# Optimization experiments

Measured on AMD Instinct MI355X. Metric: run time of the kernel, lower is better.

## Reference

```python
import jax, jax.numpy as jnp
import numpy as np

N = 50000      # nodes
E = 800000     # edges (avg degree 16)
IN_DIM = 128
H = 8          # num_heads
D = 16         # out_dim per head


def setup_inputs() -> dict:
    key = jax.random.key(0)
    ks = jax.random.split(key, 10)
    s = 1.0 / np.sqrt(IN_DIM)
    return {
        "h_src": jax.random.normal(ks[0], (N, IN_DIM), jnp.float32),
        "h_dst": jax.random.normal(ks[1], (N, IN_DIM), jnp.float32),
        "src": jax.random.randint(ks[2], (E,), 0, N),
        "dst": jax.random.randint(ks[3], (E,), 0, N),
        "Qw": jax.random.normal(ks[4], (IN_DIM, H * D), jnp.float32) * s,
        "Qb": jnp.zeros((H * D,), jnp.float32),
        "Kw": jax.random.normal(ks[5], (IN_DIM, H * D), jnp.float32) * s,
        "Kb": jnp.zeros((H * D,), jnp.float32),
        "Vw": jax.random.normal(ks[6], (IN_DIM, H * D), jnp.float32) * s,
        "Vb": jnp.zeros((H * D,), jnp.float32),
    }


def reference(h_src, h_dst, src, dst, Qw, Qb, Kw, Kb, Vw, Vb):
    # Node-level projections: [N, H, D]
    Q = (h_dst @ Qw + Qb).reshape(-1, H, D)
    K = (h_src @ Kw + Kb).reshape(-1, H, D)
    V = (h_src @ Vw + Vb).reshape(-1, H, D)
    # Edge-wise dot product per head: [E, H, 1]
    score = jnp.sum(K[src] * Q[dst], axis=-1, keepdims=True)
    # exp of clamped scaled score (note: clamp(-5,5) BEFORE exp, as in scaled_exp)
    score = jnp.exp(jnp.clip(score / jnp.float32(np.sqrt(D)), -5.0, 5.0))
    # Scatter-sum aggregation onto destination nodes
    wV = jax.ops.segment_sum(score * V[src], dst, num_segments=N)  # [N, H, D]
    z = jax.ops.segment_sum(score, dst, num_segments=N)            # [N, H, 1]
    return wV / z
```

## Files before the change

kernel.cpp:

```cpp
#include <hip/hip_runtime.h>
#include <hip/hip_bf16.h>
#include <math.h>

#define N_NODES 50000
#define E_EDGES 800000
#define IN_DIM  128
#define HD      128
#define SQRT_D_INV 0.25f

#define HIST_BLOCKS 1024
#define PROJ_BLOCKS ((N_NODES + 63) / 64)

typedef __attribute__((ext_vector_type(8))) short short8v;
typedef __attribute__((ext_vector_type(4))) float float4v;

__device__ inline unsigned short f2bf(float x) {
    __hip_bfloat16 b = __float2bfloat16(x);
    return *reinterpret_cast<unsigned short*>(&b);
}
__device__ inline float bflo(unsigned int u) { return __uint_as_float(u << 16); }
__device__ inline float bfhi(unsigned int u) { return __uint_as_float(u & 0xffff0000u); }

__global__ __launch_bounds__(256) void wtr_init_kernel(
    const float* __restrict__ Qw, const float* __restrict__ Kw, const float* __restrict__ Vw,
    unsigned short* __restrict__ wt, int* __restrict__ counts8)
{
    int i = blockIdx.x * 256 + threadIdx.x;
    for (int j = i; j <= 8 * N_NODES; j += 392 * 256) counts8[j] = 0;
    if (i < 3 * 16384) {
        int which = i >> 14;
        int r = i & 16383;
        int k = r >> 7, n = r & 127;
        const float* W = (which == 0) ? Qw : (which == 1) ? Kw : Vw;
        wt[((size_t)which << 14) + n * 128 + k] = f2bf(W[r]);
    }
}

__global__ __launch_bounds__(256) void proj_hist_kernel(
    const float* __restrict__ h_src, const float* __restrict__ h_dst,
    const unsigned short* __restrict__ wt,
    const float* __restrict__ Qb, const float* __restrict__ Kb, const float* __restrict__ Vb,
    unsigned short* __restrict__ qkv,
    const int* __restrict__ dst, int* __restrict__ counts8, int* __restrict__ rank)
{
    if (blockIdx.x < HIST_BLOCKS) {
        const int c = blockIdx.x & 7;
        int* cnt = counts8 + c * N_NODES;
        int tid = blockIdx.x * 256 + threadIdx.x;
        for (int e = tid; e < E_EDGES; e += HIST_BLOCKS * 256)
            rank[e] = atomicAdd(&cnt[dst[e]], 1);
        return;
    }

    __shared__ __align__(16) unsigned short smem[16384];
    const int t  = threadIdx.x;
    const int wv = t >> 6;
    const int l  = t & 63;
    const int lr = l & 15;
    const int kg = l >> 4;
    const int m_base = (blockIdx.x - HIST_BLOCKS) * 64 + wv * 16;
    const int arow = min(m_base + lr, N_NODES - 1);

    const float* pd = h_dst + (size_t)arow * IN_DIM;
    const float* ps = h_src + (size_t)arow * IN_DIM;

    short8v afd[4], afs[4];
    #pragma unroll
    for (int ks = 0; ks < 4; ++ks) {
        const int k0 = ks * 32 + kg * 8;
        float4 a0 = *(const float4*)&pd[k0];
        float4 a1 = *(const float4*)&pd[k0 + 4];
        float4 b0 = *(const float4*)&ps[k0];
        float4 b1 = *(const float4*)&ps[k0 + 4];
        afd[ks][0] = (short)f2bf(a0.x); afd[ks][1] = (short)f2bf(a0.y);
        afd[ks][2] = (short)f2bf(a0.z); afd[ks][3] = (short)f2bf(a0.w);
        afd[ks][4] = (short)f2bf(a1.x); afd[ks][5] = (short)f2bf(a1.y);
        afd[ks][6] = (short)f2bf(a1.z); afd[ks][7] = (short)f2bf(a1.w);
        afs[ks][0] = (short)f2bf(b0.x); afs[ks][1] = (short)f2bf(b0.y);
        afs[ks][2] = (short)f2bf(b0.z); afs[ks][3] = (short)f2bf(b0.w);
        afs[ks][4] = (short)f2bf(b1.x); afs[ks][5] = (short)f2bf(b1.y);
        afs[ks][6] = (short)f2bf(b1.z); afs[ks][7] = (short)f2bf(b1.w);
    }

    unsigned short* stg = &smem[wv * 2176];

    #pragma unroll
    for (int phase = 0; phase < 3; ++phase) {
        if (phase) __syncthreads();
        const unsigned short* wsrc = wt + ((size_t)phase << 14);
        #pragma unroll
        for (int j = 0; j < 8; ++j) {
            const int selem = j * 2048 + t * 8;
            const int d = selem * 2;
            const int sd = d ^ (((d >> 8) & 15) << 4);
            *(short8v*)((char*)smem + sd) = *(const short8v*)&wsrc[selem];
        }
        __syncthreads();

        const short8v* aF = (phase == 0) ? afd : afs;
        float4v acc[8];
        #pragma unroll
        for (int i = 0; i < 8; ++i) acc[i] = (float4v)0.f;
        #pragma unroll
        for (int ks = 0; ks < 4; ++ks) {
            short8v bf[8];
            #pragma unroll
            for (int nf = 0; nf < 8; ++nf) {
                const int a = (nf * 16 + lr) * 256 + ks * 64 + kg * 16;
                const int sa = a ^ (lr << 4);
                bf[nf] = *(const short8v*)((const char*)smem + sa);
            }
            #pragma unroll
            for (int nf = 0; nf < 8; ++nf)
                acc[nf] = __builtin_amdgcn_mfma_f32_16x16x32_bf16(aF[ks], bf[nf], acc[nf], 0, 0, 0);
        }
        __syncthreads();

        const float* bias = (phase == 0) ? Qb : (phase == 1) ? Kb : Vb;
        #pragma unroll
        for (int nf = 0; nf < 8; ++nf) {
            const float b = bias[nf * 16 + lr];
            #pragma unroll
            for (int r = 0; r < 4; ++r)
                stg[(kg * 4 + r) * 136 + nf * 16 + lr] = f2bf(acc[nf][r] + b);
        }
        #pragma unroll
        for (int i = 0; i < 4; ++i) {
            const int chunk = i * 64 + l;
            const int row = chunk >> 4;
            const int c   = (chunk & 15) * 8;
            const int m = m_base + row;
            short8v v = *(const short8v*)&stg[row * 136 + c];
            if (m < N_NODES) *(short8v*)&qkv[(size_t)m * 384 + phase * 128 + c] = v;
        }
    }
}

__global__ __launch_bounds__(256) void offsets_kernel(const int* __restrict__ counts8,
                                                      int* __restrict__ begc,
                                                      int* __restrict__ begn,
                                                      int* __restrict__ cntn,
                                                      int* __restrict__ total) {
    int n = blockIdx.x * blockDim.x + threadIdx.x;
    int lane = threadIdx.x & 63;
    int pre[8];
    int s = 0;
    if (n < N_NODES) {
        #pragma unroll
        for (int c = 0; c < 8; ++c) {
            int v = counts8[c * N_NODES + n];
            pre[c] = s; s += v;
        }
    }
    int incl = s;
    #pragma unroll
    for (int off = 1; off < 64; off <<= 1) {
        int y = __shfl_up(incl, off);
        if (lane >= off) incl += y;
    }
    int wsum = __shfl(incl, 63);
    int base = 0;
    if (lane == 0) base = atomicAdd(total, wsum);
    base = __shfl(base, 0);
    int b = base + incl - s;
    if (n < N_NODES) {
        begn[n] = b; cntn[n] = s;
        #pragma unroll
        for (int c = 0; c < 8; ++c) begc[c * N_NODES + n] = b + pre[c];
    }
}

__global__ void scatter_kernel(const int* __restrict__ src, const int* __restrict__ dst,
                               const int* __restrict__ begc, const int* __restrict__ rank,
                               int* __restrict__ esrc) {
    int e = blockIdx.x * blockDim.x + threadIdx.x;
    if (e < E_EDGES) {
        int c = (e >> 8) & 7;
        esrc[begc[c * N_NODES + dst[e]] + rank[e]] = src[e];
    }
}

__global__ __launch_bounds__(256) void agg_kernel(
    const unsigned short* __restrict__ qkv,
    const int* __restrict__ begp, const int* __restrict__ cntp,
    const int* __restrict__ esrc, float* __restrict__ out)
{
    int wave = (blockIdx.x * blockDim.x + threadIdx.x) >> 6;
    const int lane = threadIdx.x & 63;
    if (wave >= N_NODES) return;
    const int n = __builtin_amdgcn_readfirstlane(wave);
    const int e = lane >> 4;
    const int u = lane & 15;

    const uint4 qv = *(const uint4*)&qkv[(size_t)n * 384 + u * 8];
    const float q0 = bflo(qv.x), q1 = bfhi(qv.x), q2 = bflo(qv.y), q3 = bfhi(qv.y);
    const float q4 = bflo(qv.z), q5 = bfhi(qv.z), q6 = bflo(qv.w), q7 = bfhi(qv.w);

    const int b0 = begp[n], c0 = cntp[n], endp = b0 + c0;

    float a0=0.f,a1=0.f,a2=0.f,a3=0.f,a4=0.f,a5=0.f,a6=0.f,a7=0.f, z=0.f;

    for (int base = b0; base < endp; base += 16) {
        int idx[4];
        uint4 kk[4], vv[4];
        #pragma unroll
        for (int j = 0; j < 4; ++j) {
            idx[j] = base + j * 4 + e;
            const int s = esrc[min(idx[j], endp - 1)];
            const size_t ro = (size_t)s * 384;
            kk[j] = *(const uint4*)&qkv[ro + 128 + u * 8];
            vv[j] = *(const uint4*)&qkv[ro + 256 + u * 8];
        }
        #pragma unroll
        for (int j = 0; j < 4; ++j) {
            float d =      q0 * bflo(kk[j].x);
            d = fmaf(q1, bfhi(kk[j].x), d);
            d = fmaf(q2, bflo(kk[j].y), d);
            d = fmaf(q3, bfhi(kk[j].y), d);
            d = fmaf(q4, bflo(kk[j].z), d);
            d = fmaf(q5, bfhi(kk[j].z), d);
            d = fmaf(q6, bflo(kk[j].w), d);
            d = fmaf(q7, bfhi(kk[j].w), d);
            d += __shfl_xor(d, 1);
            float w = (idx[j] < endp) ? __expf(fminf(fmaxf(d * SQRT_D_INV, -5.f), 5.f)) : 0.f;
            z += w;
            a0 = fmaf(w, bflo(vv[j].x), a0);
            a1 = fmaf(w, bfhi(vv[j].x), a1);
            a2 = fmaf(w, bflo(vv[j].y), a2);
            a3 = fmaf(w, bfhi(vv[j].y), a3);
            a4 = fmaf(w, bflo(vv[j].z), a4);
            a5 = fmaf(w, bfhi(vv[j].z), a5);
            a6 = fmaf(w, bflo(vv[j].w), a6);
            a7 = fmaf(w, bfhi(vv[j].w), a7);
        }
    }

    #pragma unroll
    for (int mask = 16; mask <= 32; mask <<= 1) {
        z  += __shfl_xor(z, mask);
        a0 += __shfl_xor(a0, mask);
        a1 += __shfl_xor(a1, mask);
        a2 += __shfl_xor(a2, mask);
        a3 += __shfl_xor(a3, mask);
        a4 += __shfl_xor(a4, mask);
        a5 += __shfl_xor(a5, mask);
        a6 += __shfl_xor(a6, mask);
        a7 += __shfl_xor(a7, mask);
    }

    const float inv = 1.f / z;
    if (e == 0) {
        *(float4*)&out[(size_t)n * HD + u * 8]     = make_float4(a0*inv, a1*inv, a2*inv, a3*inv);
        *(float4*)&out[(size_t)n * HD + u * 8 + 4] = make_float4(a4*inv, a5*inv, a6*inv, a7*inv);
    }
}

extern "C" void kernel_launch(void* const* d_in, const int* in_sizes, int n_in,
                              void* d_out, int out_size, void* d_ws, size_t ws_size,
                              hipStream_t stream) {
    const float* h_src = (const float*)d_in[0];
    const float* h_dst = (const float*)d_in[1];
    const int*   src   = (const int*)d_in[2];
    const int*   dst   = (const int*)d_in[3];
    const float* Qw    = (const float*)d_in[4];
    const float* Qb    = (const float*)d_in[5];
    const float* Kw    = (const float*)d_in[6];
    const float* Kb    = (const float*)d_in[7];
    const float* Vw    = (const float*)d_in[8];
    const float* Vb    = (const float*)d_in[9];
    float* out = (float*)d_out;

    char* ws = (char*)d_ws;
    const size_t qkv_bytes = (size_t)N_NODES * 384 * sizeof(unsigned short);
    const size_t wt_bytes  = 3 * 128 * 128 * sizeof(unsigned short);
    unsigned short* qkvp = (unsigned short*)(ws);
    unsigned short* wtp  = (unsigned short*)(ws + qkv_bytes);
    int* counts8 = (int*)(ws + qkv_bytes + wt_bytes);
    int* total   = counts8 + 8 * N_NODES;
    int* begc    = counts8 + 8 * N_NODES + 1;
    int* begn    = begc + 8 * N_NODES;
    int* cntn    = begn + N_NODES;
    int* rank    = cntn + N_NODES;
    int* esrc    = rank + E_EDGES;

    wtr_init_kernel<<<392, 256, 0, stream>>>(Qw, Kw, Vw, wtp, counts8);

    proj_hist_kernel<<<HIST_BLOCKS + PROJ_BLOCKS, 256, 0, stream>>>(
        h_src, h_dst, wtp, Qb, Kb, Vb, qkvp, dst, counts8, rank);

    offsets_kernel<<<(N_NODES + 255) / 256, 256, 0, stream>>>(counts8, begc, begn, cntn, total);

    scatter_kernel<<<(E_EDGES + 255) / 256, 256, 0, stream>>>(src, dst, begc, rank, esrc);

    agg_kernel<<<(N_NODES * 64 + 255) / 256, 256, 0, stream>>>(qkvp, begn, cntn, esrc, out);
}
```

Measured before the change: 138.1 us.

## Split Q/K/V projection phases across separate blocks instead of one block looping

Each projection block now computes only one of Q, K or V for its 64-row tile, tripling the projection grid instead of looping over three phases inside one block. This removes the serial phase loop and its extra barriers, adds parallelism and lets weight loads for different matrices overlap across blocks. In exchange, h_src rows are loaded twice (once each by the K and V blocks), and more blocks must be scheduled alongside the histogram blocks.

```diff
diff --git a/kernel.cpp b/kernel.cpp
--- a/kernel.cpp
+++ b/kernel.cpp
@@ -9,7 +9,8 @@
 #define SQRT_D_INV 0.25f
 
 #define HIST_BLOCKS 1024
-#define PROJ_BLOCKS ((N_NODES + 63) / 64)
+#define NT_TILES    ((N_NODES + 63) / 64)
+#define PROJ_BLOCKS (NT_TILES * 3)
 
 typedef __attribute__((ext_vector_type(8))) short short8v;
 typedef __attribute__((ext_vector_type(4))) float float4v;
@@ -53,86 +54,77 @@
     }
 
     __shared__ __align__(16) unsigned short smem[16384];
+    const int pb    = blockIdx.x - HIST_BLOCKS;
+    const int which = pb % 3;
+    const int tile  = pb / 3;
     const int t  = threadIdx.x;
     const int wv = t >> 6;
     const int l  = t & 63;
     const int lr = l & 15;
     const int kg = l >> 4;
-    const int m_base = (blockIdx.x - HIST_BLOCKS) * 64 + wv * 16;
+    const int m_base = tile * 64 + wv * 16;
     const int arow = min(m_base + lr, N_NODES - 1);
 
-    const float* pd = h_dst + (size_t)arow * IN_DIM;
-    const float* ps = h_src + (size_t)arow * IN_DIM;
-
-    short8v afd[4], afs[4];
+    const float* A  = (which == 0) ? h_dst : h_src;
+    const float* ap = A + (size_t)arow * IN_DIM;
+
+    short8v af[4];
     #pragma unroll
     for (int ks = 0; ks < 4; ++ks) {
         const int k0 = ks * 32 + kg * 8;
-        float4 a0 = *(const float4*)&pd[k0];
-        float4 a1 = *(const float4*)&pd[k0 + 4];
-        float4 b0 = *(const float4*)&ps[k0];
-        float4 b1 = *(const float4*)&ps[k0 + 4];
-        afd[ks][0] = (short)f2bf(a0.x); afd[ks][1] = (short)f2bf(a0.y);
-        afd[ks][2] = (short)f2bf(a0.z); afd[ks][3] = (short)f2bf(a0.w);
-        afd[ks][4] = (short)f2bf(a1.x); afd[ks][5] = (short)f2bf(a1.y);
-        afd[ks][6] = (short)f2bf(a1.z); afd[ks][7] = (short)f2bf(a1.w);
-        afs[ks][0] = (short)f2bf(b0.x); afs[ks][1] = (short)f2bf(b0.y);
-        afs[ks][2] = (short)f2bf(b0.z); afs[ks][3] = (short)f2bf(b0.w);
-        afs[ks][4] = (short)f2bf(b1.x); afs[ks][5] = (short)f2bf(b1.y);
-        afs[ks][6] = (short)f2bf(b1.z); afs[ks][7] = (short)f2bf(b1.w);
-    }
-
+        float4 a0 = *(const float4*)&ap[k0];
+        float4 a1 = *(const float4*)&ap[k0 + 4];
+        af[ks][0] = (short)f2bf(a0.x); af[ks][1] = (short)f2bf(a0.y);
+        af[ks][2] = (short)f2bf(a0.z); af[ks][3] = (short)f2bf(a0.w);
+        af[ks][4] = (short)f2bf(a1.x); af[ks][5] = (short)f2bf(a1.y);
+        af[ks][6] = (short)f2bf(a1.z); af[ks][7] = (short)f2bf(a1.w);
+    }
+
+    const unsigned short* wsrc = wt + ((size_t)which << 14);
+    #pragma unroll
+    for (int j = 0; j < 8; ++j) {
+        const int selem = j * 2048 + t * 8;
+        const int d = selem * 2;
+        const int sd = d ^ (((d >> 8) & 15) << 4);
+        *(short8v*)((char*)smem + sd) = *(const short8v*)&wsrc[selem];
+    }
+    __syncthreads();
+
+    float4v acc[8];
+    #pragma unroll
+    for (int i = 0; i < 8; ++i) acc[i] = (float4v)0.f;
+    #pragma unroll
+    for (int ks = 0; ks < 4; ++ks) {
+        short8v bf[8];
+        #pragma unroll
+        for (int nf = 0; nf < 8; ++nf) {
+            const int a = (nf * 16 + lr) * 256 + ks * 64 + kg * 16;
+            const int sa = a ^ (lr << 4);
+            bf[nf] = *(const short8v*)((const char*)smem + sa);
+        }
+        #pragma unroll
+        for (int nf = 0; nf < 8; ++nf)
+            acc[nf] = __builtin_amdgcn_mfma_f32_16x16x32_bf16(af[ks], bf[nf], acc[nf], 0, 0, 0);
+    }
+    __syncthreads();
+
+    const float* bias = (which == 0) ? Qb : (which == 1) ? Kb : Vb;
     unsigned short* stg = &smem[wv * 2176];
-
-    #pragma unroll
-    for (int phase = 0; phase < 3; ++phase) {
-        if (phase) __syncthreads();
-        const unsigned short* wsrc = wt + ((size_t)phase << 14);
-        #pragma unroll
-        for (int j = 0; j < 8; ++j) {
-            const int selem = j * 2048 + t * 8;
-            const int d = selem * 2;
-            const int sd = d ^ (((d >> 8) & 15) << 4);
-            *(short8v*)((char*)smem + sd) = *(const short8v*)&wsrc[selem];
-        }
-        __syncthreads();
-
-        const short8v* aF = (phase == 0) ? afd : afs;
-        float4v acc[8];
-        #pragma unroll
-        for (int i = 0; i < 8; ++i) acc[i] = (float4v)0.f;
-        #pragma unroll
-        for (int ks = 0; ks < 4; ++ks) {
-            short8v bf[8];
-            #pragma unroll
-            for (int nf = 0; nf < 8; ++nf) {
-                const int a = (nf * 16 + lr) * 256 + ks * 64 + kg * 16;
-                const int sa = a ^ (lr << 4);
-                bf[nf] = *(const short8v*)((const char*)smem + sa);
-            }
-            #pragma unroll
-            for (int nf = 0; nf < 8; ++nf)
-                acc[nf] = __builtin_amdgcn_mfma_f32_16x16x32_bf16(aF[ks], bf[nf], acc[nf], 0, 0, 0);
-        }
-        __syncthreads();
-
-        const float* bias = (phase == 0) ? Qb : (phase == 1) ? Kb : Vb;
-        #pragma unroll
-        for (int nf = 0; nf < 8; ++nf) {
-            const float b = bias[nf * 16 + lr];
-            #pragma unroll
-            for (int r = 0; r < 4; ++r)
-                stg[(kg * 4 + r) * 136 + nf * 16 + lr] = f2bf(acc[nf][r] + b);
-        }
-        #pragma unroll
-        for (int i = 0; i < 4; ++i) {
-            const int chunk = i * 64 + l;
-            const int row = chunk >> 4;
-            const int c   = (chunk & 15) * 8;
-            const int m = m_base + row;
-            short8v v = *(const short8v*)&stg[row * 136 + c];
-            if (m < N_NODES) *(short8v*)&qkv[(size_t)m * 384 + phase * 128 + c] = v;
-        }
+    #pragma unroll
+    for (int nf = 0; nf < 8; ++nf) {
+        const float b = bias[nf * 16 + lr];
+        #pragma unroll
+        for (int r = 0; r < 4; ++r)
+            stg[(kg * 4 + r) * 136 + nf * 16 + lr] = f2bf(acc[nf][r] + b);
+    }
+    #pragma unroll
+    for (int i = 0; i < 4; ++i) {
+        const int chunk = i * 64 + l;
+        const int row = chunk >> 4;
+        const int c   = (chunk & 15) * 8;
+        const int m = m_base + row;
+        short8v v = *(const short8v*)&stg[row * 136 + c];
+        if (m < N_NODES) *(short8v*)&qkv[(size_t)m * 384 + which * 128 + c] = v;
     }
 }
 
```

After: 139.4 us. Within noise of the previous version (+0.9%).
